# Performance work log

Hardware: AMD Instinct MI355X
Metric: run time of the kernel (lower is better)

Reference implementation:

```python
import jax, jax.numpy as jnp
import numpy as np

DIM_T = 128
N_USER = 50000
N_ITEM = 50000
E = 600000
D_USER = 64
D_ITEM = 32
D_HID = 256
N_IN_USER = 25000
N_IN_ITEM = 25000
N_LAYERS = 2


def timestep_embedding(t, dim, max_period=10000.0):
    # improved-diffusion sinusoidal embedding: [cos | sin]
    half = dim // 2
    freqs = jnp.exp(-jnp.log(jnp.asarray(max_period, jnp.float32)) * jnp.arange(half, dtype=jnp.float32) / half)
    args = t.astype(jnp.float32)[:, None] * freqs  # [N, half]
    return jnp.concatenate([jnp.cos(args), jnp.sin(args)], axis=-1)


def sage_conv(x_src, x_dst, src, dst, W_nbr, W_root, b, n_dst):
    # PyG SAGEConv (aggr='mean'): lin_l(mean_j x_src[j]) + lin_r(x_dst)
    summed = jax.ops.segment_sum(x_src[src], dst, num_segments=n_dst)  # gather + scatter-add
    cnt = jax.ops.segment_sum(jnp.ones(src.shape, x_src.dtype), dst, num_segments=n_dst)
    mean = summed / jnp.maximum(cnt, 1.0)[:, None]
    return mean @ W_nbr + x_dst @ W_root + b


def mlp3(x, W1, b1, W2, b2, W3, b3):
    # rtdl baseline MLP: Linear->ReLU (x2) -> head Linear (dropout=0)
    h = jax.nn.relu(x @ W1 + b1)
    h = jax.nn.relu(h @ W2 + b2)
    return h @ W3 + b3


def _forward(x_user, x_item, t_user, t_item, e_ui_src, e_ui_dst, e_iu_src, e_iu_dst,
             te_W1, te_b1, te_W2, te_b2, proj_Wu, proj_bu, proj_Wi, proj_bi,
             sage_Wnbr, sage_Wroot, sage_b,
             mlp_u_W1, mlp_u_b1, mlp_u_W2, mlp_u_b2, mlp_u_W3, mlp_u_b3,
             mlp_i_W1, mlp_i_b1, mlp_i_W2, mlp_i_b2, mlp_i_W3, mlp_i_b3):
    def time_mlp(t):
        e = timestep_embedding(t, DIM_T)
        return jax.nn.silu(e @ te_W1 + te_b1) @ te_W2 + te_b2

    h_u = x_user @ proj_Wu + proj_bu + time_mlp(t_user)
    h_i = x_item @ proj_Wi + proj_bi + time_mlp(t_item)

    for l in range(N_LAYERS):  # loop over structurally distinct layers only
        new_i = sage_conv(h_u, h_i, e_ui_src, e_ui_dst, sage_Wnbr[l, 0], sage_Wroot[l, 0], sage_b[l, 0], N_ITEM)
        new_u = sage_conv(h_i, h_u, e_iu_src, e_iu_dst, sage_Wnbr[l, 1], sage_Wroot[l, 1], sage_b[l, 1], N_USER)
        h_u, h_i = jax.nn.relu(new_u), jax.nn.relu(new_i)

    out_u = mlp3(h_u[:N_IN_USER], mlp_u_W1, mlp_u_b1, mlp_u_W2, mlp_u_b2, mlp_u_W3, mlp_u_b3)
    out_i = mlp3(h_i[:N_IN_ITEM], mlp_i_W1, mlp_i_b1, mlp_i_W2, mlp_i_b2, mlp_i_W3, mlp_i_b3)
    return out_u, out_i


def setup_inputs() -> dict:
    key = jax.random.key(0)
    ks = iter(jax.random.split(key, 40))
    s = 0.02

    def W(shape):
        return jax.random.normal(next(ks), shape, jnp.float32) * s

    def zb(n):
        return jnp.zeros((n,), jnp.float32)

    inp = {}
    inp["x_user"] = jax.random.normal(next(ks), (N_USER, D_USER), jnp.float32)
    inp["x_item"] = jax.random.normal(next(ks), (N_ITEM, D_ITEM), jnp.float32)
    inp["t_user"] = jax.random.randint(next(ks), (N_USER,), 0, 1000, jnp.int32)
    inp["t_item"] = jax.random.randint(next(ks), (N_ITEM,), 0, 1000, jnp.int32)
    inp["e_ui_src"] = jax.random.randint(next(ks), (E,), 0, N_USER, jnp.int32)
    inp["e_ui_dst"] = jax.random.randint(next(ks), (E,), 0, N_ITEM, jnp.int32)
    inp["e_iu_src"] = jax.random.randint(next(ks), (E,), 0, N_ITEM, jnp.int32)
    inp["e_iu_dst"] = jax.random.randint(next(ks), (E,), 0, N_USER, jnp.int32)
    inp["te_W1"] = W((DIM_T, DIM_T)); inp["te_b1"] = zb(DIM_T)
    inp["te_W2"] = W((DIM_T, DIM_T)); inp["te_b2"] = zb(DIM_T)
    inp["proj_Wu"] = W((D_USER, DIM_T)); inp["proj_bu"] = zb(DIM_T)
    inp["proj_Wi"] = W((D_ITEM, DIM_T)); inp["proj_bi"] = zb(DIM_T)
    inp["sage_Wnbr"] = W((N_LAYERS, 2, DIM_T, DIM_T))   # [layer, edge_type(0:u->i,1:i->u), C, C]
    inp["sage_Wroot"] = W((N_LAYERS, 2, DIM_T, DIM_T))
    inp["sage_b"] = jnp.zeros((N_LAYERS, 2, DIM_T), jnp.float32)
    inp["mlp_u_W1"] = W((DIM_T, D_HID)); inp["mlp_u_b1"] = zb(D_HID)
    inp["mlp_u_W2"] = W((D_HID, D_HID)); inp["mlp_u_b2"] = zb(D_HID)
    inp["mlp_u_W3"] = W((D_HID, D_USER)); inp["mlp_u_b3"] = zb(D_USER)
    inp["mlp_i_W1"] = W((DIM_T, D_HID)); inp["mlp_i_b1"] = zb(D_HID)
    inp["mlp_i_W2"] = W((D_HID, D_HID)); inp["mlp_i_b2"] = zb(D_HID)
    inp["mlp_i_W3"] = W((D_HID, D_ITEM)); inp["mlp_i_b3"] = zb(D_ITEM)
    return inp


def reference(x_user, x_item, t_user, t_item, e_ui_src, e_ui_dst, e_iu_src, e_iu_dst,
              te_W1, te_b1, te_W2, te_b2, proj_Wu, proj_bu, proj_Wi, proj_bi,
              sage_Wnbr, sage_Wroot, sage_b,
              mlp_u_W1, mlp_u_b1, mlp_u_W2, mlp_u_b2, mlp_u_W3, mlp_u_b3,
              mlp_i_W1, mlp_i_b1, mlp_i_W2, mlp_i_b2, mlp_i_W3, mlp_i_b3):
    return _forward(x_user, x_item, t_user, t_item, e_ui_src, e_ui_dst, e_iu_src, e_iu_dst,
                    te_W1, te_b1, te_W2, te_b2, proj_Wu, proj_bu, proj_Wi, proj_bi,
                    sage_Wnbr, sage_Wroot, sage_b,
                    mlp_u_W1, mlp_u_b1, mlp_u_W2, mlp_u_b2, mlp_u_W3, mlp_u_b3,
                    mlp_i_W1, mlp_i_b1, mlp_i_W2, mlp_i_b2, mlp_i_W3, mlp_i_b3)
```

## Files before the change

kernel.cpp:

```cpp
#include <hip/hip_runtime.h>
#include <math.h>

#define NEDGE 600000
#define NUSER 50000
#define NITEM 50000
#define DIMT  128
#define NIN   25000
#define NTVAL 1000

typedef unsigned short ushort_t;
typedef __attribute__((ext_vector_type(8))) short bf16x8;
typedef __attribute__((ext_vector_type(8))) unsigned short us8;
typedef __attribute__((ext_vector_type(4))) float f32x4;
typedef __attribute__((ext_vector_type(4))) unsigned upk4;

__device__ __forceinline__ unsigned pack_hl(float f) {
    unsigned u = __float_as_uint(f);
    unsigned r = u + 0x7fffu + ((u >> 16) & 1u);
    unsigned h = (r >> 16) & 0xffffu;
    float fh = __uint_as_float(h << 16);
    float fl = f - fh;
    unsigned ul = __float_as_uint(fl);
    unsigned rl = ul + 0x7fffu + ((ul >> 16) & 1u);
    return h | (rl & 0xffff0000u);
}
__device__ __forceinline__ void split_bf16(float f, ushort_t& h, ushort_t& l) {
    unsigned p = pack_hl(f);
    h = (ushort_t)(p & 0xffffu);
    l = (ushort_t)(p >> 16);
}
__device__ __forceinline__ float upk_val(unsigned u) {
    return __uint_as_float(u << 16) + __uint_as_float(u & 0xffff0000u);
}

__device__ __forceinline__ void unpack_frag(upk4 p0, upk4 p1, bf16x8& ah, bf16x8& al) {
    upk4 h, l;
#if __has_builtin(__builtin_amdgcn_perm)
    h.x = __builtin_amdgcn_perm(p0.y, p0.x, 0x05040100u);
    h.y = __builtin_amdgcn_perm(p0.w, p0.z, 0x05040100u);
    h.z = __builtin_amdgcn_perm(p1.y, p1.x, 0x05040100u);
    h.w = __builtin_amdgcn_perm(p1.w, p1.z, 0x05040100u);
    l.x = __builtin_amdgcn_perm(p0.y, p0.x, 0x07060302u);
    l.y = __builtin_amdgcn_perm(p0.w, p0.z, 0x07060302u);
    l.z = __builtin_amdgcn_perm(p1.y, p1.x, 0x07060302u);
    l.w = __builtin_amdgcn_perm(p1.w, p1.z, 0x07060302u);
#else
    h.x = (p0.x & 0xffffu) | (p0.y << 16);
    h.y = (p0.z & 0xffffu) | (p0.w << 16);
    h.z = (p1.x & 0xffffu) | (p1.y << 16);
    h.w = (p1.z & 0xffffu) | (p1.w << 16);
    l.x = (p0.x >> 16) | (p0.y & 0xffff0000u);
    l.y = (p0.z >> 16) | (p0.w & 0xffff0000u);
    l.z = (p1.x >> 16) | (p1.y & 0xffff0000u);
    l.w = (p1.z >> 16) | (p1.w & 0xffff0000u);
#endif
    ah = __builtin_bit_cast(bf16x8, h);
    al = __builtin_bit_cast(bf16x8, l);
}

__device__ __forceinline__ size_t sm_addr(int row, int k, int nr) {
    return ((size_t)(k >> 4) * (unsigned)nr + (unsigned)row) * 16 + (k & 15);
}

struct WDesc { const float* src; int K; int N; unsigned dst; };
struct WDescs { WDesc d[16]; };

#define PREP_LUT  500
#define PREP_CVTW 256
#define PREP_CVTX 512
#define HIST_CH   64
#define PREP_HIST (8 * HIST_CH)
#define DRANGE    (NUSER / 8)

__global__ __launch_bounds__(256) void prep_kernel(
        WDescs wd, ushort_t* __restrict__ WT,
        const float* __restrict__ teW1, const float* __restrict__ teb1,
        const float* __restrict__ teW2, const float* __restrict__ teb2,
        float* __restrict__ Tlut,
        const float* __restrict__ xu, const float* __restrict__ xi,
        unsigned* __restrict__ xup, unsigned* __restrict__ xip,
        const int* __restrict__ s0, const int* __restrict__ d0,
        const int* __restrict__ s1, const int* __restrict__ d1,
        unsigned* __restrict__ pe0, unsigned* __restrict__ pe1,
        int* __restrict__ cnt2) {
    __shared__ float sE[2][128];
    __shared__ float sH[2][128];
    int b = blockIdx.x;
    int tid = threadIdx.x;
    if (b < PREP_LUT) {
        int r = tid >> 7, j = tid & 127;
        int t = b * 2 + r;
        {
            int jj = j & 63;
            const float Lf = 9.210340371976184f;
            float p  = -Lf * (float)jj;
            float ae = p * 0.015625f;
            float freq = (float)exp((double)ae);
            float arg  = (float)t * freq;
            double a = (double)arg;
            sE[r][j] = (j < 64) ? (float)cos(a) : (float)sin(a);
        }
        __syncthreads();
        {
            float acc = teb1[j];
            for (int k = 0; k < 128; ++k) acc = fmaf(sE[r][k], teW1[k * 128 + j], acc);
            float s = 1.f / (1.f + expf(-acc));
            sH[r][j] = acc * s;
        }
        __syncthreads();
        {
            float acc = teb2[j];
            for (int k = 0; k < 128; ++k) acc = fmaf(sH[r][k], teW2[k * 128 + j], acc);
            Tlut[(size_t)t * 128 + j] = acc;
        }
    } else if (b < PREP_LUT + PREP_CVTW) {
        int g = (b - PREP_LUT) * 256 + tid;
        int gs = PREP_CVTW * 256;
#pragma unroll 1
        for (int i = 0; i < 16; ++i) {
            const WDesc w = wd.d[i];
            int sz = w.K * w.N;
            int ng = sz >> 3;
            int kshift = 31 - __clz(w.K);
            int kmask = w.K - 1;
            ushort_t* ph = WT + w.dst;
            ushort_t* pl = ph + sz;
            for (int t = g; t < ng; t += gs) {
                int e8 = t << 3;
                int n  = e8 >> kshift;
                int k0 = e8 & kmask;
                us8 hb, lb;
#pragma unroll
                for (int j = 0; j < 8; ++j) {
                    ushort_t h, l;
                    split_bf16(w.src[(size_t)(k0 + j) * w.N + n], h, l);
                    hb[j] = h; lb[j] = l;
                }
                *reinterpret_cast<us8*>(ph + e8) = hb;
                *reinterpret_cast<us8*>(pl + e8) = lb;
            }
        }
    } else if (b < PREP_LUT + PREP_CVTW + PREP_CVTX) {
        int g = (b - PREP_LUT - PREP_CVTW) * 256 + tid;
        int gs = PREP_CVTX * 256;
        for (int i = g; i < NUSER * 64; i += gs) {
            int row = i >> 6, k = i & 63;
            xup[sm_addr(row, k, NUSER)] = pack_hl(xu[i]);
        }
        for (int i = g; i < NITEM * 32; i += gs) {
            int row = i >> 5, k = i & 31;
            xip[sm_addr(row, k, NITEM)] = pack_hl(xi[i]);
        }
        for (int i = g; i < NEDGE; i += gs) {
            pe0[i] = ((unsigned)d0[i] & 0xffffu) | ((unsigned)s0[i] << 16);
            pe1[i] = ((unsigned)d1[i] & 0xffffu) | ((unsigned)s1[i] << 16);
        }
    } else {
        int hb = b - PREP_LUT - PREP_CVTW - PREP_CVTX;
        int r = hb & 7, c = hb >> 3;
        int lo = r * DRANGE, hi = lo + DRANGE;
        const int epb = (NEDGE + HIST_CH - 1) / HIST_CH;
        int e0 = c * epb, e1 = min(e0 + epb, NEDGE);
        for (int e = e0 + tid; e < e1; e += 256) {
            int d = d0[e];
            if (d >= lo && d < hi) atomicAdd(&cnt2[d], 1);
        }
        for (int e = e0 + tid; e < e1; e += 256) {
            int d = d1[e];
            if (d >= lo && d < hi) atomicAdd(&cnt2[NUSER + d], 1);
        }
    }
}

#define ACT_NONE 0
#define ACT_RELU 1

struct MProb {
    const unsigned *A1p; int K1;
    const unsigned *A2p; int K2;
    const ushort_t *W1, *W2;
    const float* bias; const float* res; const int* tidx;
    float* Yf; unsigned* Yp;
    int M; int nblk; int anr; int ynr;
};

template<int NOUT, int ACT, bool DUAL, int RESMODE, int OUTMODE>
__global__ __launch_bounds__(256)
void mgemm_kernel(MProb q0, MProb q1) {
    constexpr int WN  = (NOUT >= 64) ? 64 : NOUT;
    constexpr int NWC = NOUT / WN;
    constexpr int NWR = 4 / NWC;
    constexpr int BM  = NWR * 64;
    constexpr int NF  = WN / 16;

    const bool firstp = (blockIdx.x < (unsigned)q0.nblk);
    const MProb& q = firstp ? q0 : q1;
    const int bid = firstp ? blockIdx.x : (blockIdx.x - q0.nblk);

    const int w    = threadIdx.x >> 6;
    const int lane = threadIdx.x & 63;
    const int wc   = w % NWC;
    const int wr   = w / NWC;
    const int mw   = bid * BM + wr * 64;
    const int nw   = wc * WN;
    const int lr   = lane & 15;
    const int lkg  = lane >> 4;

    f32x4 acc[4][NF];
#pragma unroll
    for (int i = 0; i < 4; ++i)
#pragma unroll
        for (int j = 0; j < NF; ++j) acc[i][j] = (f32x4)0.f;

    const int nkt1 = q.K1 / 32;
    const int nkt  = nkt1 + (DUAL ? q.K2 / 32 : 0);

    upk4 pa[4][2];
    auto loadA = [&](int kt) {
        const unsigned* Ap; int kk;
        if (!DUAL || kt < nkt1) { Ap = q.A1p; kk = kt * 32; }
        else                    { Ap = q.A2p; kk = (kt - nkt1) * 32; }
        const int kb = kk + lkg * 8;
#pragma unroll
        for (int mf = 0; mf < 4; ++mf) {
            int row = mw + mf * 16 + lr;
            if (row < q.M) {
                const upk4* p = reinterpret_cast<const upk4*>(Ap + sm_addr(row, kb, q.anr));
                pa[mf][0] = p[0]; pa[mf][1] = p[1];
            } else {
                pa[mf][0] = (upk4)0u; pa[mf][1] = (upk4)0u;
            }
        }
    };

    loadA(0);
#pragma unroll 1
    for (int kt = 0; kt < nkt; ++kt) {
        bf16x8 a_h[4], a_l[4];
#pragma unroll
        for (int mf = 0; mf < 4; ++mf) unpack_frag(pa[mf][0], pa[mf][1], a_h[mf], a_l[mf]);
        if (kt + 1 < nkt) loadA(kt + 1);

        const ushort_t* Wh; int K, kk;
        if (!DUAL || kt < nkt1) { Wh = q.W1; K = q.K1; kk = kt * 32; }
        else                    { Wh = q.W2; K = q.K2; kk = (kt - nkt1) * 32; }
        const ushort_t* Wl = Wh + (size_t)NOUT * K;
        const int kb = kk + lkg * 8;
        bf16x8 b_h[NF], b_l[NF];
#pragma unroll
        for (int nf = 0; nf < NF; ++nf) {
            int col = nw + nf * 16 + lr;
            b_h[nf] = *reinterpret_cast<const bf16x8*>(Wh + (size_t)col * K + kb);
            b_l[nf] = *reinterpret_cast<const bf16x8*>(Wl + (size_t)col * K + kb);
        }
#pragma unroll
        for (int mf = 0; mf < 4; ++mf)
#pragma unroll
            for (int nf = 0; nf < NF; ++nf) {
                acc[mf][nf] = __builtin_amdgcn_mfma_f32_16x16x32_bf16(a_h[mf], b_h[nf], acc[mf][nf], 0, 0, 0);
                acc[mf][nf] = __builtin_amdgcn_mfma_f32_16x16x32_bf16(a_h[mf], b_l[nf], acc[mf][nf], 0, 0, 0);
                acc[mf][nf] = __builtin_amdgcn_mfma_f32_16x16x32_bf16(a_l[mf], b_h[nf], acc[mf][nf], 0, 0, 0);
            }
    }

    __syncthreads();

    float bcol[NF];
#pragma unroll
    for (int nf = 0; nf < NF; ++nf) bcol[nf] = q.bias[nw + nf * 16 + lr];

#pragma unroll
    for (int mf = 0; mf < 4; ++mf) {
#pragma unroll
        for (int r = 0; r < 4; ++r) {
            int row = mw + mf * 16 + lkg * 4 + r;
            if (row >= q.M) continue;
            const float* rp = nullptr;
            if (RESMODE == 2) { int tv = q.tidx[row]; rp = q.res + (size_t)tv * NOUT; }
#pragma unroll
            for (int nf = 0; nf < NF; ++nf) {
                int col = nw + nf * 16 + lr;
                float v = acc[mf][nf][r] + bcol[nf];
                if (RESMODE == 2) v += rp[col];
                if (ACT == ACT_RELU) v = fmaxf(v, 0.f);
                if (OUTMODE & 1) q.Yf[(size_t)row * NOUT + col] = v;
                if (OUTMODE & 2) q.Yp[sm_addr(row, col, q.ynr)] = pack_hl(v);
            }
        }
    }
}

#define SCAN_CHUNK 2048
#define GSCAN 25

__global__ __launch_bounds__(256) void scan1x2_kernel(const int* __restrict__ cnt2,
                                                      int* __restrict__ bsum2) {
    __shared__ int sdata[256];
    int p = blockIdx.x / GSCAN, b = blockIdx.x % GSCAN;
    const int* cnt = cnt2 + p * NUSER;
    int base = b * SCAN_CHUNK + threadIdx.x * 8;
    int s = 0;
#pragma unroll
    for (int j = 0; j < 8; ++j) { int i = base + j; if (i < NUSER) s += cnt[i]; }
    sdata[threadIdx.x] = s;
    __syncthreads();
    for (int st = 128; st > 0; st >>= 1) {
        if ((int)threadIdx.x < st) sdata[threadIdx.x] += sdata[threadIdx.x + st];
        __syncthreads();
    }
    if (threadIdx.x == 0) bsum2[p * 32 + b] = sdata[0];
}

__global__ __launch_bounds__(256) void scan3x2_kernel(const int* __restrict__ cnt2,
                                                      const int* __restrict__ bsum2,
                                                      int* __restrict__ off_ui,
                                                      int* __restrict__ off_iu,
                                                      int* __restrict__ wp2) {
    __shared__ int sth[256];
    int p = blockIdx.x / GSCAN, b = blockIdx.x % GSCAN;
    const int* cnt = cnt2 + p * NUSER;
    int* offs = p ? off_iu : off_ui;
    int* wp = wp2 + p * NUSER;
    int t = threadIdx.x;
    int boff = 0;
    for (int i = 0; i < b; ++i) boff += bsum2[p * 32 + i];
    int base = b * SCAN_CHUNK + t * 8;
    int loc[8];
    int s = 0;
#pragma unroll
    for (int j = 0; j < 8; ++j) {
        int i = base + j;
        int v = (i < NUSER) ? cnt[i] : 0;
        loc[j] = s; s += v;
    }
    sth[t] = s;
    __syncthreads();
    for (int st = 1; st < 256; st <<= 1) {
        int v = (t >= st) ? sth[t - st] : 0;
        __syncthreads();
        sth[t] += v;
        __syncthreads();
    }
    int exc = (t == 0) ? 0 : sth[t - 1];
#pragma unroll
    for (int j = 0; j < 8; ++j) {
        int i = base + j;
        if (i < NUSER) { int o = boff + exc + loc[j]; offs[i] = o; wp[i] = o; }
    }
    if (b == GSCAN - 1 && t == 255) offs[NUSER] = boff + sth[255];
}

#define FILL_CH 256

__global__ __launch_bounds__(256) void fill2p_kernel(
        const unsigned* __restrict__ pe0, const unsigned* __restrict__ pe1,
        int* __restrict__ wp2,
        ushort_t* __restrict__ bkt0, ushort_t* __restrict__ bkt1) {
    int r = blockIdx.x & 7, c = blockIdx.x >> 3;
    int lo = r * DRANGE, hi = lo + DRANGE;
    const int epb = (NEDGE + FILL_CH - 1) / FILL_CH;
    int e0 = c * epb, e1 = min(e0 + epb, NEDGE);
#pragma unroll 4
    for (int e = e0 + (int)threadIdx.x; e < e1; e += 256) {
        unsigned p = pe0[e];
        int d = (int)(p & 0xffffu);
        if (d >= lo && d < hi) { int pos = atomicAdd(&wp2[d], 1); bkt0[pos] = (ushort_t)(p >> 16); }
    }
#pragma unroll 4
    for (int e = e0 + (int)threadIdx.x; e < e1; e += 256) {
        unsigned p = pe1[e];
        int d = (int)(p & 0xffffu);
        if (d >= lo && d < hi) { int pos = atomicAdd(&wp2[NUSER + d], 1); bkt1[pos] = (ushort_t)(p >> 16); }
    }
}

struct GProb { const unsigned* Hp; const int* offs; const ushort_t* bkt; unsigned* Op; int N; };
#define GCH64 782

__global__ __launch_bounds__(256)
void gather_slice4_kernel(GProb g0, GProb g1) {
    int s = blockIdx.x & 7;
    int chunk = blockIdx.x >> 3;
    int grp = threadIdx.x >> 2;
    int c   = threadIdx.x & 3;
    const bool firstp = (chunk < GCH64);
    const GProb& g = firstp ? g0 : g1;
    int row = (firstp ? chunk : chunk - GCH64) * 64 + grp;
    if (row >= g.N) return;
    int beg = g.offs[row], end = g.offs[row + 1];
    const upk4* __restrict__ base =
        reinterpret_cast<const upk4*>(g.Hp + ((size_t)s * NUSER) * 16) + c;
    float s0 = 0.f, s1 = 0.f, s2 = 0.f, s3 = 0.f;
    int e = beg;
    for (; e + 1 < end; e += 2) {
        int r0 = g.bkt[e], r1 = g.bkt[e + 1];
        upk4 v0 = base[(size_t)r0 * 4];
        upk4 v1 = base[(size_t)r1 * 4];
        s0 += upk_val(v0.x) + upk_val(v1.x);
        s1 += upk_val(v0.y) + upk_val(v1.y);
        s2 += upk_val(v0.z) + upk_val(v1.z);
        s3 += upk_val(v0.w) + upk_val(v1.w);
    }
    if (e < end) {
        upk4 v = base[(size_t)g.bkt[e] * 4];
        s0 += upk_val(v.x); s1 += upk_val(v.y);
        s2 += upk_val(v.z); s3 += upk_val(v.w);
    }
    float d = (float)max(end - beg, 1);
    upk4 o;
    o.x = pack_hl(s0 / d); o.y = pack_hl(s1 / d);
    o.z = pack_hl(s2 / d); o.w = pack_hl(s3 / d);
    *(reinterpret_cast<upk4*>(g.Op + ((size_t)s * NUSER + row) * 16) + c) = o;
}

extern "C" void kernel_launch(void* const* d_in, const int* in_sizes, int n_in,
                              void* d_out, int out_size, void* d_ws, size_t ws_size,
                              hipStream_t stream) {
    const float* x_user  = (const float*)d_in[0];
    const float* x_item  = (const float*)d_in[1];
    const int*   t_user  = (const int*)d_in[2];
    const int*   t_item  = (const int*)d_in[3];
    const int*   eui_src = (const int*)d_in[4];
    const int*   eui_dst = (const int*)d_in[5];
    const int*   eiu_src = (const int*)d_in[6];
    const int*   eiu_dst = (const int*)d_in[7];
    const float* te_W1 = (const float*)d_in[8];  const float* te_b1 = (const float*)d_in[9];
    const float* te_W2 = (const float*)d_in[10]; const float* te_b2 = (const float*)d_in[11];
    const float* proj_Wu = (const float*)d_in[12]; const float* proj_bu = (const float*)d_in[13];
    const float* proj_Wi = (const float*)d_in[14]; const float* proj_bi = (const float*)d_in[15];
    const float* sage_Wnbr  = (const float*)d_in[16];
    const float* sage_Wroot = (const float*)d_in[17];
    const float* sage_b     = (const float*)d_in[18];
    const float* mu_W1 = (const float*)d_in[19]; const float* mu_b1 = (const float*)d_in[20];
    const float* mu_W2 = (const float*)d_in[21]; const float* mu_b2 = (const float*)d_in[22];
    const float* mu_W3 = (const float*)d_in[23]; const float* mu_b3 = (const float*)d_in[24];
    const float* mi_W1 = (const float*)d_in[25]; const float* mi_b1 = (const float*)d_in[26];
    const float* mi_W2 = (const float*)d_in[27]; const float* mi_b2 = (const float*)d_in[28];
    const float* mi_W3 = (const float*)d_in[29]; const float* mi_b3 = (const float*)d_in[30];

    float* out_u = (float*)d_out;
    float* out_i = out_u + (size_t)NIN * 64;

    const size_t PL = (size_t)NUSER * DIMT;
    float* Tlut = (float*)d_ws;
    unsigned* up = (unsigned*)(Tlut + NTVAL * 128);
    unsigned* Hp_u = up;
    unsigned* Hp_i = up + PL;
    unsigned* G0   = up + 2 * PL;
    unsigned* Gp_i = G0;
    unsigned* Gp_u = G0 + PL;
    ushort_t* WT   = (ushort_t*)(up + 4 * PL);

    WDescs wd;
    unsigned woff[16];
    unsigned off = 0; int wi = 0;
    auto addw = [&](const float* src, int K, int N) {
        wd.d[wi].src = src; wd.d[wi].K = K; wd.d[wi].N = N; wd.d[wi].dst = off;
        woff[wi] = off; off += 2u * K * N; ++wi;
    };
    addw(proj_Wu, 64, 128);
    addw(proj_Wi, 32, 128);
    for (int l = 0; l < 2; ++l)
        for (int e = 0; e < 2; ++e)
            addw(sage_Wnbr + (size_t)(l * 2 + e) * DIMT * DIMT, 128, 128);
    for (int l = 0; l < 2; ++l)
        for (int e = 0; e < 2; ++e)
            addw(sage_Wroot + (size_t)(l * 2 + e) * DIMT * DIMT, 128, 128);
    addw(mu_W1, 128, 256);
    addw(mu_W2, 256, 256);
    addw(mu_W3, 256, 64);
    addw(mi_W1, 128, 256);
    addw(mi_W2, 256, 256);
    addw(mi_W3, 256, 32);

    int* ip = (int*)(WT + off + (off & 1));
    int* cnt2   = ip;  ip += 2 * NUSER;
    int* wp2    = ip;  ip += 2 * NUSER;
    int* off_ui = ip;  ip += NUSER + 1;
    int* off_iu = ip;  ip += NUSER + 1;
    int* bsum2  = ip;  ip += 64;
    unsigned* pe0 = (unsigned*)ip;  ip += NEDGE;
    unsigned* pe1 = (unsigned*)ip;  ip += NEDGE;
    ushort_t* bkt_ui = (ushort_t*)ip;
    ushort_t* bkt_iu = bkt_ui + NEDGE;

    MProb qn = {}; qn.nblk = 0;

    unsigned* xu_p = G0;
    unsigned* xi_p = G0 + PL;

    hipMemsetAsync(cnt2, 0, 2 * NUSER * sizeof(int), stream);
    prep_kernel<<<PREP_LUT + PREP_CVTW + PREP_CVTX + PREP_HIST, 256, 0, stream>>>(
        wd, WT, te_W1, te_b1, te_W2, te_b2, Tlut,
        x_user, x_item, xu_p, xi_p,
        eui_src, eui_dst, eiu_src, eiu_dst, pe0, pe1, cnt2);

    scan1x2_kernel<<<2 * GSCAN, 256, 0, stream>>>(cnt2, bsum2);
    scan3x2_kernel<<<2 * GSCAN, 256, 0, stream>>>(cnt2, bsum2, off_ui, off_iu, wp2);
    fill2p_kernel<<<8 * FILL_CH, 256, 0, stream>>>(pe0, pe1, wp2, bkt_ui, bkt_iu);

    {
        MProb qu = {}; MProb qi = {};
        qu.A1p = xu_p; qu.K1 = 64;
        qu.W1 = WT + woff[0]; qu.bias = proj_bu; qu.res = Tlut; qu.tidx = t_user;
        qu.Yp = Hp_u; qu.M = NUSER; qu.nblk = (NUSER + 127) / 128;
        qu.anr = NUSER; qu.ynr = NUSER;
        qi.A1p = xi_p; qi.K1 = 32;
        qi.W1 = WT + woff[1]; qi.bias = proj_bi; qi.res = Tlut; qi.tidx = t_item;
        qi.Yp = Hp_i; qi.M = NITEM; qi.nblk = (NITEM + 127) / 128;
        qi.anr = NITEM; qi.ynr = NITEM;
        mgemm_kernel<128, ACT_NONE, false, 2, 2><<<qu.nblk + qi.nblk, 256, 0, stream>>>(qu, qi);
    }

    for (int l = 0; l < 2; ++l) {
        {
            GProb gi = { Hp_u, off_ui, bkt_ui, Gp_i, NITEM };
            GProb gu = { Hp_i, off_iu, bkt_iu, Gp_u, NUSER };
            gather_slice4_kernel<<<8 * 2 * GCH64, 256, 0, stream>>>(gi, gu);
        }
        {
            MProb qi = {}; MProb qu = {};
            qi.A1p = Gp_i; qi.K1 = 128;
            qi.A2p = Hp_i; qi.K2 = 128;
            qi.W1 = WT + woff[2 + l * 2 + 0]; qi.W2 = WT + woff[6 + l * 2 + 0];
            qi.bias = sage_b + (size_t)(l * 2 + 0) * DIMT;
            qi.Yp = Hp_i; qi.M = NITEM; qi.nblk = (NITEM + 127) / 128;
            qi.anr = NUSER; qi.ynr = NUSER;
            qu.A1p = Gp_u; qu.K1 = 128;
            qu.A2p = Hp_u; qu.K2 = 128;
            qu.W1 = WT + woff[2 + l * 2 + 1]; qu.W2 = WT + woff[6 + l * 2 + 1];
            qu.bias = sage_b + (size_t)(l * 2 + 1) * DIMT;
            qu.Yp = Hp_u; qu.M = NUSER; qu.nblk = (NUSER + 127) / 128;
            qu.anr = NUSER; qu.ynr = NUSER;
            mgemm_kernel<128, ACT_RELU, true, 0, 2><<<qi.nblk + qu.nblk, 256, 0, stream>>>(qi, qu);
        }
    }

    unsigned* Tp_u = G0;
    unsigned* Tp_i = G0 + PL;
    {
        MProb qu = {}; MProb qi = {};
        qu.A1p = Hp_u; qu.K1 = 128;
        qu.W1 = WT + woff[10]; qu.bias = mu_b1;
        qu.Yp = Tp_u; qu.M = NIN; qu.nblk = (NIN + 63) / 64;
        qu.anr = NUSER; qu.ynr = NIN;
        qi.A1p = Hp_i; qi.K1 = 128;
        qi.W1 = WT + woff[13]; qi.bias = mi_b1;
        qi.Yp = Tp_i; qi.M = NIN; qi.nblk = (NIN + 63) / 64;
        qi.anr = NUSER; qi.ynr = NIN;
        mgemm_kernel<256, ACT_RELU, false, 0, 2><<<qu.nblk + qi.nblk, 256, 0, stream>>>(qu, qi);
    }
    {
        MProb qu = {}; MProb qi = {};
        qu.A1p = Tp_u; qu.K1 = 256;
        qu.W1 = WT + woff[11]; qu.bias = mu_b2;
        qu.Yp = Tp_u; qu.M = NIN; qu.nblk = (NIN + 63) / 64;
        qu.anr = NIN; qu.ynr = NIN;
        qi.A1p = Tp_i; qi.K1 = 256;
        qi.W1 = WT + woff[14]; qi.bias = mi_b2;
        qi.Yp = Tp_i; qi.M = NIN; qi.nblk = (NIN + 63) / 64;
        qi.anr = NIN; qi.ynr = NIN;
        mgemm_kernel<256, ACT_RELU, false, 0, 2><<<qu.nblk + qi.nblk, 256, 0, stream>>>(qu, qi);
    }
    {
        MProb q = {};
        q.A1p = Tp_u; q.K1 = 256;
        q.W1 = WT + woff[12]; q.bias = mu_b3;
        q.Yf = out_u; q.M = NIN; q.nblk = (NIN + 255) / 256;
        q.anr = NIN; q.ynr = NIN;
        mgemm_kernel<64, ACT_NONE, false, 0, 1><<<q.nblk, 256, 0, stream>>>(q, qn);
    }
    {
        MProb q = {};
        q.A1p = Tp_i; q.K1 = 256;
        q.W1 = WT + woff[15]; q.bias = mi_b3;
        q.Yf = out_i; q.M = NIN; q.nblk = (NIN + 255) / 256;
        q.anr = NIN; q.ynr = NIN;
        mgemm_kernel<32, ACT_NONE, false, 0, 1><<<q.nblk, 256, 0, stream>>>(q, qn);
    }

    (void)in_sizes; (void)n_in; (void)out_size; (void)ws_size;
}
```

Before: 515.9 us.

## Unroll gather loop by four, split LUT MLP accumulators, widen histogram chunks

```diff
diff --git a/kernel.cpp b/kernel.cpp
--- a/kernel.cpp
+++ b/kernel.cpp
@@ -68,7 +68,7 @@
 #define PREP_LUT  500
 #define PREP_CVTW 256
 #define PREP_CVTX 512
-#define HIST_CH   64
+#define HIST_CH   256
 #define PREP_HIST (8 * HIST_CH)
 #define DRANGE    (NUSER / 8)
 
@@ -102,16 +102,27 @@
         }
         __syncthreads();
         {
-            float acc = teb1[j];
-            for (int k = 0; k < 128; ++k) acc = fmaf(sE[r][k], teW1[k * 128 + j], acc);
+            float a0 = 0.f, a1 = 0.f, a2 = 0.f, a3 = 0.f;
+            for (int k = 0; k < 128; k += 4) {
+                a0 = fmaf(sE[r][k],     teW1[(k)     * 128 + j], a0);
+                a1 = fmaf(sE[r][k + 1], teW1[(k + 1) * 128 + j], a1);
+                a2 = fmaf(sE[r][k + 2], teW1[(k + 2) * 128 + j], a2);
+                a3 = fmaf(sE[r][k + 3], teW1[(k + 3) * 128 + j], a3);
+            }
+            float acc = teb1[j] + ((a0 + a1) + (a2 + a3));
             float s = 1.f / (1.f + expf(-acc));
             sH[r][j] = acc * s;
         }
         __syncthreads();
         {
-            float acc = teb2[j];
-            for (int k = 0; k < 128; ++k) acc = fmaf(sH[r][k], teW2[k * 128 + j], acc);
-            Tlut[(size_t)t * 128 + j] = acc;
+            float a0 = 0.f, a1 = 0.f, a2 = 0.f, a3 = 0.f;
+            for (int k = 0; k < 128; k += 4) {
+                a0 = fmaf(sH[r][k],     teW2[(k)     * 128 + j], a0);
+                a1 = fmaf(sH[r][k + 1], teW2[(k + 1) * 128 + j], a1);
+                a2 = fmaf(sH[r][k + 2], teW2[(k + 2) * 128 + j], a2);
+                a3 = fmaf(sH[r][k + 3], teW2[(k + 3) * 128 + j], a3);
+            }
+            Tlut[(size_t)t * 128 + j] = teb2[j] + ((a0 + a1) + (a2 + a3));
         }
     } else if (b < PREP_LUT + PREP_CVTW) {
         int g = (b - PREP_LUT) * 256 + tid;
@@ -374,8 +385,20 @@
     }
 }
 
-struct GProb { const unsigned* Hp; const int* offs; const ushort_t* bkt; unsigned* Op; int N; };
+struct GProb { const unsigned* Hp; const int* offs; const ushort_t* bkt;
+               unsigned* Op; int N; };
 #define GCH64 782
+
+__device__ __forceinline__ void gacc(float4& a, upk4 v) {
+    a.x += __uint_as_float(v.x << 16);
+    a.y += __uint_as_float(v.y << 16);
+    a.z += __uint_as_float(v.z << 16);
+    a.w += __uint_as_float(v.w << 16);
+    a.x += __uint_as_float(v.x & 0xffff0000u);
+    a.y += __uint_as_float(v.y & 0xffff0000u);
+    a.z += __uint_as_float(v.z & 0xffff0000u);
+    a.w += __uint_as_float(v.w & 0xffff0000u);
+}
 
 __global__ __launch_bounds__(256)
 void gather_slice4_kernel(GProb g0, GProb g1) {
@@ -390,26 +413,21 @@
     int beg = g.offs[row], end = g.offs[row + 1];
     const upk4* __restrict__ base =
         reinterpret_cast<const upk4*>(g.Hp + ((size_t)s * NUSER) * 16) + c;
-    float s0 = 0.f, s1 = 0.f, s2 = 0.f, s3 = 0.f;
+    float4 a = make_float4(0.f, 0.f, 0.f, 0.f);
     int e = beg;
-    for (; e + 1 < end; e += 2) {
-        int r0 = g.bkt[e], r1 = g.bkt[e + 1];
+    for (; e + 3 < end; e += 4) {
+        int r0 = g.bkt[e], r1 = g.bkt[e + 1], r2 = g.bkt[e + 2], r3 = g.bkt[e + 3];
         upk4 v0 = base[(size_t)r0 * 4];
         upk4 v1 = base[(size_t)r1 * 4];
-        s0 += upk_val(v0.x) + upk_val(v1.x);
-        s1 += upk_val(v0.y) + upk_val(v1.y);
-        s2 += upk_val(v0.z) + upk_val(v1.z);
-        s3 += upk_val(v0.w) + upk_val(v1.w);
-    }
-    if (e < end) {
-        upk4 v = base[(size_t)g.bkt[e] * 4];
-        s0 += upk_val(v.x); s1 += upk_val(v.y);
-        s2 += upk_val(v.z); s3 += upk_val(v.w);
-    }
+        upk4 v2 = base[(size_t)r2 * 4];
+        upk4 v3 = base[(size_t)r3 * 4];
+        gacc(a, v0); gacc(a, v1); gacc(a, v2); gacc(a, v3);
+    }
+    for (; e < end; ++e) gacc(a, base[(size_t)g.bkt[e] * 4]);
     float d = (float)max(end - beg, 1);
     upk4 o;
-    o.x = pack_hl(s0 / d); o.y = pack_hl(s1 / d);
-    o.z = pack_hl(s2 / d); o.w = pack_hl(s3 / d);
+    o.x = pack_hl(a.x / d); o.y = pack_hl(a.y / d);
+    o.z = pack_hl(a.z / d); o.w = pack_hl(a.w / d);
     *(reinterpret_cast<upk4*>(g.Op + ((size_t)s * NUSER + row) * 16) + c) = o;
 }
 
```

Result: faster. 498.9 us (-3.3%).
